# Kernel optimization log

Hardware: AMD Instinct MI355X
Metric: run time of the kernel (lower is better)

The kernel has to match this reference:

```python
import jax, jax.numpy as jnp
import numpy as np

H = 16          # num_attention_heads
GRID = 16       # crop_size // patch_size
TOK_PER_FRAME = GRID * GRID


def _rope(x, pos, dim):
    # x: (B,H,N,dim), pos: (N,) int positions
    half = dim // 2
    omega = jnp.arange(half, dtype=x.dtype) / (dim / 2.0)
    inv = 1.0 / (10000.0 ** omega)                      # (half,)
    freq = pos.astype(x.dtype)[:, None] * inv            # (N, half)
    sin = jnp.concatenate([jnp.sin(freq), jnp.sin(freq)], axis=-1)  # (N, dim)  (tile, per source)
    cos = jnp.concatenate([jnp.cos(freq), jnp.cos(freq)], axis=-1)
    y = x.reshape(*x.shape[:-1], half, 2)
    y1, y2 = y[..., 0], y[..., 1]
    rot = jnp.stack((-y2, y1), axis=-1).reshape(x.shape)  # interleaved rotate-pairs
    return x * cos + rot * sin


def _apply_3d_rope(qk, f_ids, h_ids, w_ids, d_dim):
    s = 0
    parts = []
    for pos in (f_ids, h_ids, w_ids):
        parts.append(_rope(qk[..., s:s + d_dim], pos, d_dim))
        s += d_dim
    if s < qk.shape[-1]:
        parts.append(qk[..., s:])
    return jnp.concatenate(parts, axis=-1)


def setup_inputs() -> dict:
    key = jax.random.key(0)
    ks = jax.random.split(key, 5)
    D = 1024
    B, N = 4, 2048
    sc = 0.02
    return {
        "hidden_states": jax.random.normal(ks[0], (B, N, D), jnp.float32),
        "Wq": jax.random.normal(ks[1], (D, D), jnp.float32) * sc,
        "bq": jnp.zeros((D,), jnp.float32),
        "Wk": jax.random.normal(ks[2], (D, D), jnp.float32) * sc,
        "bk": jnp.zeros((D,), jnp.float32),
        "Wv": jax.random.normal(ks[3], (D, D), jnp.float32) * sc,
        "bv": jnp.zeros((D,), jnp.float32),
        "Wo": jax.random.normal(ks[4], (D, D), jnp.float32) * sc,
        "bo": jnp.zeros((D,), jnp.float32),
    }


def reference(hidden_states, Wq, bq, Wk, bk, Wv, bv, Wo, bo):
    B, N, D = hidden_states.shape
    hd = D // H
    d_dim = 2 * (hd // 3 // 2)  # per-component rotary dim (20 for hd=64)

    def heads(x):  # (B,N,D) -> (B,H,N,hd)
        return x.reshape(B, N, H, hd).transpose(0, 2, 1, 3)

    q = heads(hidden_states @ Wq + bq)
    k = heads(hidden_states @ Wk + bk)
    v = heads(hidden_states @ Wv + bv)

    ids = jnp.arange(N)
    f_ids = ids // TOK_PER_FRAME
    rem = ids - TOK_PER_FRAME * f_ids
    h_ids = rem // GRID
    w_ids = rem - GRID * h_ids

    q = _apply_3d_rope(q, f_ids, h_ids, w_ids, d_dim)
    k = _apply_3d_rope(k, f_ids, h_ids, w_ids, d_dim)

    scale = hd ** -0.5
    attn = jnp.einsum('bhqd,bhkd->bhqk', q, k) * scale
    attn = jax.nn.softmax(attn.astype(jnp.float32), axis=-1).astype(q.dtype)
    ctx = jnp.einsum('bhqk,bhkd->bhqd', attn, v)
    ctx = ctx.transpose(0, 2, 1, 3).reshape(B, N, D)
    return ctx @ Wo + bo
```

## Files before the change

kernel.cpp:

```cpp
#include <hip/hip_runtime.h>
#include <stdint.h>

#define H_   16
#define NS_  2048
#define B_   4
#define DM_  1024
#define HD_  64
#define MTOT (B_*NS_)

typedef __attribute__((ext_vector_type(8)))  short bf16x8;
typedef __attribute__((ext_vector_type(4)))  float f32x4;
typedef __attribute__((ext_vector_type(16))) float f32x16;

__device__ __forceinline__ unsigned short f2bf(float f){
  union { float f; unsigned u; } v; v.f = f;
  unsigned r = v.u + 0x7FFFu + ((v.u >> 16) & 1u);
  return (unsigned short)(r >> 16);
}
__device__ __forceinline__ float bf2f(unsigned short u){
  union { unsigned u; float f; } v; v.u = ((unsigned)u) << 16;
  return v.f;
}
__device__ __forceinline__ unsigned pk2(float a, float b){
  return (unsigned)f2bf(a) | ((unsigned)f2bf(b) << 16);
}
__device__ __forceinline__ unsigned cvtpk(float a, float b){
  unsigned r;
  asm("v_cvt_pk_bf16_f32 %0, %1, %2" : "=v"(r) : "v"(a), "v"(b));
  return r;
}
__device__ __forceinline__ float exp2a(float x){
  float r;
  asm("v_exp_f32 %0, %1" : "=v"(r) : "v"(x));
  return r;
}
__device__ __forceinline__ void gll16(const void* g, void* l){
  __builtin_amdgcn_global_load_lds(
      (const __attribute__((address_space(1))) unsigned int*)g,
      (__attribute__((address_space(3))) unsigned int*)l,
      16, 0, 0);
}

__global__ void k_cast_x(const float* __restrict__ x, unsigned short* __restrict__ xb){
  long i = ((long)blockIdx.x*256 + threadIdx.x)*4;
  float4 v = *(const float4*)(x + i);
  ushort4 o; o.x=f2bf(v.x); o.y=f2bf(v.y); o.z=f2bf(v.z); o.w=f2bf(v.w);
  *(ushort4*)(xb + i) = o;
}

__global__ void k_wt4(const float* __restrict__ W0, const float* __restrict__ W1,
                      const float* __restrict__ W2, const float* __restrict__ W3,
                      unsigned short* __restrict__ T0, unsigned short* __restrict__ T1,
                      unsigned short* __restrict__ T2, unsigned short* __restrict__ T3){
  __shared__ float tile[64][65];
  const int z = blockIdx.z;
  const float* W = (z==0)? W0 : (z==1)? W1 : (z==2)? W2 : W3;
  unsigned short* Wt = (z==0)? T0 : (z==1)? T1 : (z==2)? T2 : T3;
  int kt = blockIdx.y*64, nt = blockIdx.x*64;
  int t = threadIdx.x;
  int r = t >> 4, c4 = (t & 15)*4;
#pragma unroll
  for (int i=0;i<4;i++){
    int k = r + i*16;
    float4 v = *(const float4*)(W + (size_t)(kt + k)*DM_ + nt + c4);
    tile[k][c4] = v.x; tile[k][c4+1]=v.y; tile[k][c4+2]=v.z; tile[k][c4+3]=v.w;
  }
  __syncthreads();
#pragma unroll
  for (int i=0;i<4;i++){
    int n = r + i*16;
    ushort4 o;
    o.x = f2bf(tile[c4+0][n]); o.y = f2bf(tile[c4+1][n]);
    o.z = f2bf(tile[c4+2][n]); o.w = f2bf(tile[c4+3][n]);
    *(ushort4*)(Wt + (size_t)(nt + n)*DM_ + kt + c4) = o;
  }
}

__global__ void k_tab(float2* __restrict__ tab){
  int n = blockIdx.x*64 + threadIdx.x;
  int f = n >> 8, rem = n & 255, hh = rem >> 4, ww = rem & 15;
  float pos[3]; pos[0]=(float)f; pos[1]=(float)hh; pos[2]=(float)ww;
#pragma unroll
  for (int c=0;c<3;c++)
#pragma unroll
    for (int i=0;i<10;i++){
      float inv = exp2f(-(float)i * 1.3287712379549449f);
      float s, co;
      sincosf(pos[c]*inv, &s, &co);
      tab[n*30 + c*10 + i] = make_float2(co, s);
    }
}

__global__ __launch_bounds__(256) void k_gemm_qkv(const unsigned short* __restrict__ A,
                                                  const unsigned short* __restrict__ wq,
                                                  const unsigned short* __restrict__ wk,
                                                  const unsigned short* __restrict__ wv,
                                                  const float* __restrict__ bq,
                                                  const float* __restrict__ bk,
                                                  const float* __restrict__ bv,
                                                  unsigned short* __restrict__ Qb,
                                                  unsigned short* __restrict__ Kb,
                                                  unsigned short* __restrict__ VTb)
{
  __shared__ unsigned short As[128*32];
  __shared__ unsigned short Bs[128*32];
  const int tid = threadIdx.x, lane = tid & 63, w = tid >> 6;
  const int mat = blockIdx.x >> 3;
  const int nt  = (blockIdx.x & 7)*128;
  const int mt  = blockIdx.y*128;
  const unsigned short* Wt  = (mat==0)? wq : (mat==1)? wk : wv;
  const float*          bias= (mat==0)? bq : (mat==1)? bk : bv;
  const int wm = (w >> 1)*64, wn = (w & 1)*64;
  const int qc = lane & 15, g = lane >> 4;
  f32x4 acc[4][4] = {};

  const unsigned short* gA = A  + (size_t)(mt + w*32 + (lane>>2))*DM_ + (lane&3)*8;
  const unsigned short* gB = Wt + (size_t)(nt + w*32 + (lane>>2))*DM_ + (lane&3)*8;
  unsigned short* lA = &As[(w*32)*32];
  unsigned short* lB = &Bs[(w*32)*32];

  for (int k0 = 0; k0 < DM_; k0 += 32){
    gll16(gA + k0,           lA);
    gll16(gA + k0 + 16*DM_,  lA + 16*32);
    gll16(gB + k0,           lB);
    gll16(gB + k0 + 16*DM_,  lB + 16*32);
    __syncthreads();
    bf16x8 af[4], bfr[4];
#pragma unroll
    for (int m=0;m<4;m++) af[m]  = *(const bf16x8*)&As[(wm + m*16 + qc)*32 + g*8];
#pragma unroll
    for (int n=0;n<4;n++) bfr[n] = *(const bf16x8*)&Bs[(wn + n*16 + qc)*32 + g*8];
#pragma unroll
    for (int m=0;m<4;m++)
#pragma unroll
      for (int n=0;n<4;n++)
        acc[m][n] = __builtin_amdgcn_mfma_f32_16x16x32_bf16(af[m], bfr[n], acc[m][n], 0,0,0);
    __syncthreads();
  }

  if (mat < 2){
    unsigned short* out = (mat==0)? Qb : Kb;
#pragma unroll
    for (int n=0;n<4;n++){
      int col = nt + wn + n*16 + qc;
      float bv_ = bias[col];
      int hh = col >> 6, d = col & 63;
#pragma unroll
      for (int m=0;m<4;m++){
#pragma unroll
        for (int r=0;r<4;r++){
          int mrow = mt + wm + m*16 + g*4 + r;
          size_t idx = (((size_t)(mrow >> 11)*H_ + hh)*NS_ + (mrow & (NS_-1)))*HD_ + d;
          out[idx] = f2bf(acc[m][n][r] + bv_);
        }
      }
    }
  } else {
#pragma unroll
    for (int n=0;n<4;n++){
      int col = nt + wn + n*16 + qc;
      float bv_ = bias[col];
      int hh = col >> 6, d = col & 63;
#pragma unroll
      for (int m=0;m<4;m++){
        int mrow0 = mt + wm + m*16 + g*4;
        int b = mrow0 >> 11, ntk = mrow0 & (NS_-1);
        int pos = (ntk & ~12) | ((ntk & 4) << 1) | ((ntk & 8) >> 1);
        ushort4 o;
        o.x = f2bf(acc[m][n][0] + bv_);
        o.y = f2bf(acc[m][n][1] + bv_);
        o.z = f2bf(acc[m][n][2] + bv_);
        o.w = f2bf(acc[m][n][3] + bv_);
        *(ushort4*)(VTb + (((size_t)(b*H_ + hh)*HD_ + d)*NS_ + pos)) = o;
      }
    }
  }
}

#define QSCALE 0.18033688011112042f
__global__ void k_rope(unsigned short* __restrict__ Qb, unsigned short* __restrict__ Kb,
                       const float2* __restrict__ tab)
{
  const int t = threadIdx.x;
  const int d4 = (t & 15)*4;
  const long gtok = (long)blockIdx.x*16 + (t >> 4);
  size_t base = (size_t)gtok*HD_ + d4;
  if (d4 >= 60){
    ushort4 v = *(ushort4*)(Qb + base);
    ushort4 o;
    o.x = f2bf(bf2f(v.x)*QSCALE); o.y = f2bf(bf2f(v.y)*QSCALE);
    o.z = f2bf(bf2f(v.z)*QSCALE); o.w = f2bf(bf2f(v.w)*QSCALE);
    *(ushort4*)(Qb + base) = o;
    return;
  }
  const int n = (int)(gtok & (NS_-1));
  const int c = d4 / 20;
  const int dd = d4 - c*20;
  const float2* tb = tab + n*30 + c*10;
  float2 cs0 = tb[(dd+0) % 10];
  float2 cs1 = tb[(dd+1) % 10];
  float2 cs2 = tb[(dd+2) % 10];
  float2 cs3 = tb[(dd+3) % 10];
#pragma unroll
  for (int which = 0; which < 2; which++){
    unsigned short* P = which ? Kb : Qb;
    float sc = which ? 1.f : QSCALE;
    ushort4 v = *(ushort4*)(P + base);
    float x0=bf2f(v.x), x1=bf2f(v.y), x2=bf2f(v.z), x3=bf2f(v.w);
    ushort4 o;
    o.x = f2bf((x0*cs0.x - x1*cs0.y)*sc);
    o.y = f2bf((x1*cs1.x + x0*cs1.y)*sc);
    o.z = f2bf((x2*cs2.x - x3*cs2.y)*sc);
    o.w = f2bf((x3*cs3.x + x2*cs3.y)*sc);
    *(ushort4*)(P + base) = o;
  }
}

__global__ __launch_bounds__(256, 4) void k_attn(const unsigned short* __restrict__ Q,
                                                 const unsigned short* __restrict__ K,
                                                 const unsigned short* __restrict__ VT,
                                                 unsigned short* __restrict__ ctxout)
{
  __shared__ __attribute__((aligned(16))) char smem[32768];
  const int tid  = threadIdx.x;
  const int lane = tid & 63, w = tid >> 6;
  const int qcol = lane & 31, h = lane >> 5;
  const int sw   = (lane & 7) << 4;
  const int bh   = blockIdx.x;
  const int q0   = blockIdx.y*128 + w*32;

  const unsigned short* Qp = Q  + ((size_t)bh*NS_ + q0)*HD_;
  const unsigned short* Kp = K  + (size_t)bh*NS_*HD_;
  const unsigned short* Vp = VT + (size_t)bh*HD_*NS_;

  const int trow = tid >> 3;
  const int tc   = (tid & 7) ^ (trow & 7);

  bf16x8 qf[4];
#pragma unroll
  for (int i=0;i<4;i++)
    qf[i] = *(const bf16x8*)(Qp + (size_t)qcol*HD_ + 16*i + 8*h);

  {
    const unsigned short* gk = Kp + (size_t)trow*HD_ + tc*8;
    const unsigned short* gv = Vp + (size_t)trow*NS_ + tc*8;
    gll16(gk,          smem + w*1024);
    gll16(gk + 32*HD_, smem + 4096 + w*1024);
    gll16(gv,          smem + 8192 + w*1024);
    gll16(gv + 32*NS_, smem + 8192 + 4096 + w*1024);
  }

  f32x16 ctx0 = {}, ctx1 = {};
  float mrun = -1e30f, lp = 0.f;

  for (int t = 0; t < NS_/64; ++t){
    const int curo = (t & 1) * 16384;
    __syncthreads();
    if (t + 1 < NS_/64){
      const int kb = (t+1)*64;
      const int nxt = ((t+1) & 1) * 16384;
      const unsigned short* gk = Kp + (size_t)(kb + trow)*HD_ + tc*8;
      const unsigned short* gv = Vp + (size_t)trow*NS_ + kb + tc*8;
      gll16(gk,          smem + nxt + w*1024);
      gll16(gk + 32*HD_, smem + nxt + 4096 + w*1024);
      gll16(gv,          smem + nxt + 8192 + w*1024);
      gll16(gv + 32*NS_, smem + nxt + 8192 + 4096 + w*1024);
    }
    const char* kls = smem + curo;
    const char* vls = smem + curo + 8192;

#pragma unroll
    for (int s = 0; s < 2; ++s){
      f32x16 st = {};
      __builtin_amdgcn_s_setprio(1);
#pragma unroll
      for (int i=0;i<4;i++){
        bf16x8 kf = *(const bf16x8*)(kls + ((((32*s + qcol)*128) + 32*i + 16*h) ^ sw));
        st = __builtin_amdgcn_mfma_f32_32x32x16_bf16(kf, qf[i], st, 0,0,0);
      }
      __builtin_amdgcn_s_setprio(0);
      float a0 = fmaxf(fmaxf(st[0],  st[1]),  st[2]);
      float a1 = fmaxf(fmaxf(st[3],  st[4]),  st[5]);
      float a2 = fmaxf(fmaxf(st[6],  st[7]),  st[8]);
      float a3 = fmaxf(fmaxf(st[9],  st[10]), st[11]);
      float a4 = fmaxf(fmaxf(st[12], st[13]), st[14]);
      float tm = fmaxf(fmaxf(fmaxf(a0,a1),a2), fmaxf(fmaxf(a3,a4),st[15]));
      if (!__all(tm - mrun <= 11.5f)){
        float tp = fmaxf(tm, __shfl_xor(tm, 32));
        float mnew = fmaxf(mrun, tp);
        float alpha = exp2a(mrun - mnew);
        lp *= alpha;
#pragma unroll
        for (int r=0;r<16;r++){ ctx0[r]*=alpha; ctx1[r]*=alpha; }
        mrun = mnew;
      }
      unsigned u[8];
      float ps = 0.f;
#pragma unroll
      for (int r=0;r<8;r++){
        float ea = exp2a(st[2*r]   - mrun);
        float eb = exp2a(st[2*r+1] - mrun);
        unsigned uu = cvtpk(ea, eb);
        u[r] = uu;
        union { unsigned q; float f; } lo, hi;
        lo.q = uu << 16; hi.q = uu & 0xFFFF0000u;
        ps += lo.f + hi.f;
      }
      lp += ps;
      bf16x8 pf0 = __builtin_bit_cast(bf16x8, make_uint4(u[0],u[1],u[2],u[3]));
      bf16x8 pf1 = __builtin_bit_cast(bf16x8, make_uint4(u[4],u[5],u[6],u[7]));

      __builtin_amdgcn_s_setprio(1);
#pragma unroll
      for (int kc=0; kc<2; ++kc){
        const bf16x8 pf = kc ? pf1 : pf0;
        bf16x8 vf0 = *(const bf16x8*)(vls + ((qcol)*128      + ((64*s + 32*kc + 16*h) ^ sw)));
        ctx0 = __builtin_amdgcn_mfma_f32_32x32x16_bf16(vf0, pf, ctx0, 0,0,0);
        bf16x8 vf1 = *(const bf16x8*)(vls + ((32 + qcol)*128 + ((64*s + 32*kc + 16*h) ^ sw)));
        ctx1 = __builtin_amdgcn_mfma_f32_32x32x16_bf16(vf1, pf, ctx1, 0,0,0);
      }
      __builtin_amdgcn_s_setprio(0);
    }
  }

  float lsum = lp + __shfl_xor(lp, 32);
  float linv = 1.f / lsum;
  __syncthreads();
  char* reg = smem + w*4096;
#pragma unroll
  for (int rq=0; rq<4; ++rq){
    int db0 = 8*rq + 4*h;
    uint2 v0, v1;
    v0.x = pk2(ctx0[4*rq+0]*linv, ctx0[4*rq+1]*linv);
    v0.y = pk2(ctx0[4*rq+2]*linv, ctx0[4*rq+3]*linv);
    v1.x = pk2(ctx1[4*rq+0]*linv, ctx1[4*rq+1]*linv);
    v1.y = pk2(ctx1[4*rq+2]*linv, ctx1[4*rq+3]*linv);
    *(uint2*)(reg + qcol*128 + db0*2)      = v0;
    *(uint2*)(reg + qcol*128 + (32+db0)*2) = v1;
  }
  __syncthreads();
  const int b = bh >> 4, head = bh & 15;
  unsigned short* outp = ctxout + ((size_t)b*NS_ + q0)*DM_ + head*HD_;
#pragma unroll
  for (int p=0;p<4;p++){
    int row = p*8 + (lane>>3);
    uint4 v = *(const uint4*)(reg + row*128 + (lane&7)*16);
    *(uint4*)(outp + (size_t)row*DM_ + (lane&7)*8) = v;
  }
}

__global__ __launch_bounds__(256) void k_gemm_o(const unsigned short* __restrict__ A,
                                                const unsigned short* __restrict__ Wt,
                                                const float* __restrict__ bias,
                                                float* __restrict__ out)
{
  __shared__ unsigned short As[128*32];
  __shared__ unsigned short Bs[128*32];
  const int tid = threadIdx.x, lane = tid & 63, w = tid >> 6;
  const int mt = blockIdx.y*128, nt = blockIdx.x*128;
  const int wm = (w >> 1)*64, wn = (w & 1)*64;
  const int qc = lane & 15, g = lane >> 4;
  f32x4 acc[4][4] = {};

  const unsigned short* gA = A  + (size_t)(mt + w*32 + (lane>>2))*DM_ + (lane&3)*8;
  const unsigned short* gB = Wt + (size_t)(nt + w*32 + (lane>>2))*DM_ + (lane&3)*8;
  unsigned short* lA = &As[(w*32)*32];
  unsigned short* lB = &Bs[(w*32)*32];

  for (int k0 = 0; k0 < DM_; k0 += 32){
    gll16(gA + k0,           lA);
    gll16(gA + k0 + 16*DM_,  lA + 16*32);
    gll16(gB + k0,           lB);
    gll16(gB + k0 + 16*DM_,  lB + 16*32);
    __syncthreads();
    bf16x8 af[4], bfr[4];
#pragma unroll
    for (int m=0;m<4;m++) af[m]  = *(const bf16x8*)&As[(wm + m*16 + qc)*32 + g*8];
#pragma unroll
    for (int n=0;n<4;n++) bfr[n] = *(const bf16x8*)&Bs[(wn + n*16 + qc)*32 + g*8];
#pragma unroll
    for (int m=0;m<4;m++)
#pragma unroll
      for (int n=0;n<4;n++)
        acc[m][n] = __builtin_amdgcn_mfma_f32_16x16x32_bf16(af[m], bfr[n], acc[m][n], 0,0,0);
    __syncthreads();
  }

#pragma unroll
  for (int n=0;n<4;n++){
    int col = nt + wn + n*16 + qc;
    float bv = bias[col];
#pragma unroll
    for (int m=0;m<4;m++){
#pragma unroll
      for (int r=0;r<4;r++){
        int mrow = mt + wm + m*16 + g*4 + r;
        out[(size_t)mrow*DM_ + col] = acc[m][n][r] + bv;
      }
    }
  }
}

extern "C" void kernel_launch(void* const* d_in, const int* in_sizes, int n_in,
                              void* d_out, int out_size, void* d_ws, size_t ws_size,
                              hipStream_t stream)
{
  const float* hs = (const float*)d_in[0];
  const float* Wq = (const float*)d_in[1];
  const float* bq = (const float*)d_in[2];
  const float* Wk = (const float*)d_in[3];
  const float* bk = (const float*)d_in[4];
  const float* Wv = (const float*)d_in[5];
  const float* bv = (const float*)d_in[6];
  const float* Wo = (const float*)d_in[7];
  const float* bo = (const float*)d_in[8];

  char* ws = (char*)d_ws;
  size_t off = 0;
  auto alloc = [&](size_t b){ void* p = ws + off; off += (b + 255) & ~(size_t)255; return p; };
  unsigned short* xb  = (unsigned short*)alloc((size_t)MTOT*DM_*2);
  unsigned short* wqt = (unsigned short*)alloc((size_t)DM_*DM_*2);
  unsigned short* wkt = (unsigned short*)alloc((size_t)DM_*DM_*2);
  unsigned short* wvt = (unsigned short*)alloc((size_t)DM_*DM_*2);
  unsigned short* wot = (unsigned short*)alloc((size_t)DM_*DM_*2);
  float2*         tab = (float2*)alloc((size_t)NS_*30*sizeof(float2));
  unsigned short* Qb  = (unsigned short*)alloc((size_t)MTOT*DM_*2);
  unsigned short* Kb  = (unsigned short*)alloc((size_t)MTOT*DM_*2);
  unsigned short* VTb = (unsigned short*)alloc((size_t)MTOT*DM_*2);
  unsigned short* cxb = (unsigned short*)alloc((size_t)MTOT*DM_*2);

  k_cast_x<<<dim3(MTOT*DM_/1024), dim3(256), 0, stream>>>(hs, xb);
  k_wt4<<<dim3(16,16,4), dim3(256), 0, stream>>>(Wq, Wk, Wv, Wo, wqt, wkt, wvt, wot);
  k_tab<<<dim3(32), dim3(64), 0, stream>>>(tab);

  k_gemm_qkv<<<dim3(24,64), dim3(256), 0, stream>>>(xb, wqt, wkt, wvt, bq, bk, bv,
                                                    Qb, Kb, VTb);

  k_rope<<<dim3(64*NS_/16), dim3(256), 0, stream>>>(Qb, Kb, tab);

  k_attn<<<dim3(64, 16), dim3(256), 0, stream>>>(Qb, Kb, VTb, cxb);

  k_gemm_o<<<dim3(8,64), dim3(256), 0, stream>>>(cxb, wot, bo, (float*)d_out);
}
```

Baseline: 248.0 us.

## Replace QKV and output GEMMs with a 256x256 double-buffered swizzled LDS GEMM

Replaces both 128x128, K=32 GEMM kernels with one templated 512-thread kernel. Each block computes a 256x256 tile with K-steps of 64, double-buffers 128KB of dynamic LDS using XOR-swizzled rows, and prefetches two stages ahead under explicit vmcnt waits and barriers. It also raises MFMA priority with setprio and remaps block IDs so neighbouring tiles land on the same XCD. The larger tiles cut global and LDS traffic per FLOP. In exchange, the grids are coarse (384 and 128 blocks), which risks poor CU occupancy and tail imbalance, and the 128 fp32 accumulators per thread risk register pressure or spills under the launch bounds.

Measured after the change: 240.0 us. 3.2% less time.

```diff
diff --git a/kernel.cpp b/kernel.cpp
--- a/kernel.cpp
+++ b/kernel.cpp
@@ -91,67 +91,150 @@
     }
 }
 
-__global__ __launch_bounds__(256) void k_gemm_qkv(const unsigned short* __restrict__ A,
-                                                  const unsigned short* __restrict__ wq,
-                                                  const unsigned short* __restrict__ wk,
-                                                  const unsigned short* __restrict__ wv,
-                                                  const float* __restrict__ bq,
-                                                  const float* __restrict__ bk,
-                                                  const float* __restrict__ bv,
-                                                  unsigned short* __restrict__ Qb,
-                                                  unsigned short* __restrict__ Kb,
-                                                  unsigned short* __restrict__ VTb)
+__device__ __forceinline__ void stage256(const unsigned short* __restrict__ gsrc,
+                                         char* ldst, int tid){
+  const int srow = tid >> 3;
+  const int gch  = (tid & 7) ^ (srow & 7);
+  const unsigned short* gp = gsrc + (size_t)srow*DM_ + gch*8;
+  char* lp = ldst + tid*16;
+#pragma unroll
+  for (int j=0;j<4;j++)
+    gll16(gp + (size_t)(j*64)*DM_, lp + j*8192);
+}
+
+template<int MODE>
+__global__ __launch_bounds__(512, 2) void k_gemm256(
+    const unsigned short* __restrict__ A,
+    const unsigned short* __restrict__ w0,
+    const unsigned short* __restrict__ w1,
+    const unsigned short* __restrict__ w2,
+    const float* __restrict__ b0,
+    const float* __restrict__ b1,
+    const float* __restrict__ b2,
+    unsigned short* __restrict__ Qb,
+    unsigned short* __restrict__ Kb,
+    unsigned short* __restrict__ VTb,
+    float* __restrict__ Fout)
 {
-  __shared__ unsigned short As[128*32];
-  __shared__ unsigned short Bs[128*32];
+  extern __shared__ char smem[];
+  char* aL = smem;
+  char* bL = smem + 65536;
   const int tid = threadIdx.x, lane = tid & 63, w = tid >> 6;
-  const int mat = blockIdx.x >> 3;
-  const int nt  = (blockIdx.x & 7)*128;
-  const int mt  = blockIdx.y*128;
-  const unsigned short* Wt  = (mat==0)? wq : (mat==1)? wk : wv;
-  const float*          bias= (mat==0)? bq : (mat==1)? bk : bv;
-  const int wm = (w >> 1)*64, wn = (w & 1)*64;
   const int qc = lane & 15, g = lane >> 4;
-  f32x4 acc[4][4] = {};
-
-  const unsigned short* gA = A  + (size_t)(mt + w*32 + (lane>>2))*DM_ + (lane&3)*8;
-  const unsigned short* gB = Wt + (size_t)(nt + w*32 + (lane>>2))*DM_ + (lane&3)*8;
-  unsigned short* lA = &As[(w*32)*32];
-  unsigned short* lB = &Bs[(w*32)*32];
-
-  for (int k0 = 0; k0 < DM_; k0 += 32){
-    gll16(gA + k0,           lA);
-    gll16(gA + k0 + 16*DM_,  lA + 16*32);
-    gll16(gB + k0,           lB);
-    gll16(gB + k0 + 16*DM_,  lB + 16*32);
-    __syncthreads();
-    bf16x8 af[4], bfr[4];
-#pragma unroll
-    for (int m=0;m<4;m++) af[m]  = *(const bf16x8*)&As[(wm + m*16 + qc)*32 + g*8];
-#pragma unroll
-    for (int n=0;n<4;n++) bfr[n] = *(const bf16x8*)&Bs[(wn + n*16 + qc)*32 + g*8];
+  const int wm = (w >> 2)*128, wn = (w & 3)*64;
+
+  int mat, mt, nt;
+  {
+    int id = blockIdx.x;
+    if (MODE == 0){
+      int wg = (id & 7)*48 + (id >> 3);
+      mat = wg >> 7; int rem = wg & 127;
+      mt = (rem >> 2)*256; nt = (rem & 3)*256;
+    } else {
+      int wg = (id & 7)*16 + (id >> 3);
+      mat = 0; mt = (wg >> 2)*256; nt = (wg & 3)*256;
+    }
+  }
+  const unsigned short* Wt = (MODE==1)? w0 : ((mat==0)? w0 : (mat==1)? w1 : w2);
+  const float* bias        = (MODE==1)? b0 : ((mat==0)? b0 : (mat==1)? b1 : b2);
+
+  const unsigned short* Ab = A  + (size_t)mt*DM_;
+  const unsigned short* Bb = Wt + (size_t)nt*DM_;
+
+  stage256(Ab,      aL,         tid);
+  stage256(Bb,      bL,         tid);
+  stage256(Ab + 64, aL + 32768, tid);
+  stage256(Bb + 64, bL + 32768, tid);
+
+  f32x4 acc[8][4] = {};
+
+  for (int kt = 0; kt < 16; ++kt){
+    const int bu = kt & 1;
+    if (kt < 15) asm volatile("s_waitcnt vmcnt(8)" ::: "memory");
+    else         asm volatile("s_waitcnt vmcnt(0)" ::: "memory");
+    __builtin_amdgcn_s_barrier();
+    __builtin_amdgcn_sched_barrier(0);
+    const char* aT = aL + bu*32768;
+    const char* bT = bL + bu*32768;
+
+    bf16x8 bfr[4][2], af[4][2], af2[4][2];
+#pragma unroll
+    for (int n=0;n<4;n++)
+#pragma unroll
+      for (int ks=0;ks<2;ks++){
+        int row = wn + n*16 + qc;
+        bfr[n][ks] = *(const bf16x8*)(bT + row*128 + ((ks*64 + g*16) ^ ((row&7)<<4)));
+      }
 #pragma unroll
     for (int m=0;m<4;m++)
 #pragma unroll
+      for (int ks=0;ks<2;ks++){
+        int row = wm + m*16 + qc;
+        af[m][ks] = *(const bf16x8*)(aT + row*128 + ((ks*64 + g*16) ^ ((row&7)<<4)));
+      }
+    __builtin_amdgcn_s_setprio(1);
+#pragma unroll
+    for (int m=0;m<4;m++)
+#pragma unroll
       for (int n=0;n<4;n++)
-        acc[m][n] = __builtin_amdgcn_mfma_f32_16x16x32_bf16(af[m], bfr[n], acc[m][n], 0,0,0);
-    __syncthreads();
-  }
-
-  if (mat < 2){
-    unsigned short* out = (mat==0)? Qb : Kb;
+#pragma unroll
+        for (int ks=0;ks<2;ks++)
+          acc[m][n] = __builtin_amdgcn_mfma_f32_16x16x32_bf16(af[m][ks], bfr[n][ks], acc[m][n], 0,0,0);
+    __builtin_amdgcn_s_setprio(0);
+#pragma unroll
+    for (int m=0;m<4;m++)
+#pragma unroll
+      for (int ks=0;ks<2;ks++){
+        int row = wm + 64 + m*16 + qc;
+        af2[m][ks] = *(const bf16x8*)(aT + row*128 + ((ks*64 + g*16) ^ ((row&7)<<4)));
+      }
+    asm volatile("s_waitcnt lgkmcnt(0)" ::: "memory");
+    __builtin_amdgcn_sched_barrier(0);
+    __builtin_amdgcn_s_barrier();
+    __builtin_amdgcn_sched_barrier(0);
+    if (kt < 14){
+      stage256(Ab + (size_t)(kt+2)*64, aL + bu*32768, tid);
+      stage256(Bb + (size_t)(kt+2)*64, bL + bu*32768, tid);
+    }
+    __builtin_amdgcn_s_setprio(1);
+#pragma unroll
+    for (int m=0;m<4;m++)
+#pragma unroll
+      for (int n=0;n<4;n++)
+#pragma unroll
+        for (int ks=0;ks<2;ks++)
+          acc[4+m][n] = __builtin_amdgcn_mfma_f32_16x16x32_bf16(af2[m][ks], bfr[n][ks], acc[4+m][n], 0,0,0);
+    __builtin_amdgcn_s_setprio(0);
+  }
+
+  if (MODE == 1){
 #pragma unroll
     for (int n=0;n<4;n++){
       int col = nt + wn + n*16 + qc;
-      float bv_ = bias[col];
+      float bv = bias[col];
+#pragma unroll
+      for (int m=0;m<8;m++){
+#pragma unroll
+        for (int r=0;r<4;r++){
+          int mrow = mt + wm + m*16 + g*4 + r;
+          Fout[(size_t)mrow*DM_ + col] = acc[m][n][r] + bv;
+        }
+      }
+    }
+  } else if (mat < 2){
+    unsigned short* out = (mat==0)? Qb : Kb;
+#pragma unroll
+    for (int n=0;n<4;n++){
+      int col = nt + wn + n*16 + qc;
+      float bv = bias[col];
       int hh = col >> 6, d = col & 63;
 #pragma unroll
-      for (int m=0;m<4;m++){
+      for (int m=0;m<8;m++){
 #pragma unroll
         for (int r=0;r<4;r++){
           int mrow = mt + wm + m*16 + g*4 + r;
           size_t idx = (((size_t)(mrow >> 11)*H_ + hh)*NS_ + (mrow & (NS_-1)))*HD_ + d;
-          out[idx] = f2bf(acc[m][n][r] + bv_);
+          out[idx] = f2bf(acc[m][n][r] + bv);
         }
       }
     }
@@ -159,18 +242,18 @@
 #pragma unroll
     for (int n=0;n<4;n++){
       int col = nt + wn + n*16 + qc;
-      float bv_ = bias[col];
+      float bv = bias[col];
       int hh = col >> 6, d = col & 63;
 #pragma unroll
-      for (int m=0;m<4;m++){
+      for (int m=0;m<8;m++){
         int mrow0 = mt + wm + m*16 + g*4;
         int b = mrow0 >> 11, ntk = mrow0 & (NS_-1);
         int pos = (ntk & ~12) | ((ntk & 4) << 1) | ((ntk & 8) >> 1);
         ushort4 o;
-        o.x = f2bf(acc[m][n][0] + bv_);
-        o.y = f2bf(acc[m][n][1] + bv_);
-        o.z = f2bf(acc[m][n][2] + bv_);
-        o.w = f2bf(acc[m][n][3] + bv_);
+        o.x = f2bf(acc[m][n][0] + bv);
+        o.y = f2bf(acc[m][n][1] + bv);
+        o.z = f2bf(acc[m][n][2] + bv);
+        o.w = f2bf(acc[m][n][3] + bv);
         *(ushort4*)(VTb + (((size_t)(b*H_ + hh)*HD_ + d)*NS_ + pos)) = o;
       }
     }
@@ -349,58 +432,6 @@
   }
 }
 
-__global__ __launch_bounds__(256) void k_gemm_o(const unsigned short* __restrict__ A,
-                                                const unsigned short* __restrict__ Wt,
-                                                const float* __restrict__ bias,
-                                                float* __restrict__ out)
-{
-  __shared__ unsigned short As[128*32];
-  __shared__ unsigned short Bs[128*32];
-  const int tid = threadIdx.x, lane = tid & 63, w = tid >> 6;
-  const int mt = blockIdx.y*128, nt = blockIdx.x*128;
-  const int wm = (w >> 1)*64, wn = (w & 1)*64;
-  const int qc = lane & 15, g = lane >> 4;
-  f32x4 acc[4][4] = {};
-
-  const unsigned short* gA = A  + (size_t)(mt + w*32 + (lane>>2))*DM_ + (lane&3)*8;
-  const unsigned short* gB = Wt + (size_t)(nt + w*32 + (lane>>2))*DM_ + (lane&3)*8;
-  unsigned short* lA = &As[(w*32)*32];
-  unsigned short* lB = &Bs[(w*32)*32];
-
-  for (int k0 = 0; k0 < DM_; k0 += 32){
-    gll16(gA + k0,           lA);
-    gll16(gA + k0 + 16*DM_,  lA + 16*32);
-    gll16(gB + k0,           lB);
-    gll16(gB + k0 + 16*DM_,  lB + 16*32);
-    __syncthreads();
-    bf16x8 af[4], bfr[4];
-#pragma unroll
-    for (int m=0;m<4;m++) af[m]  = *(const bf16x8*)&As[(wm + m*16 + qc)*32 + g*8];
-#pragma unroll
-    for (int n=0;n<4;n++) bfr[n] = *(const bf16x8*)&Bs[(wn + n*16 + qc)*32 + g*8];
-#pragma unroll
-    for (int m=0;m<4;m++)
-#pragma unroll
-      for (int n=0;n<4;n++)
-        acc[m][n] = __builtin_amdgcn_mfma_f32_16x16x32_bf16(af[m], bfr[n], acc[m][n], 0,0,0);
-    __syncthreads();
-  }
-
-#pragma unroll
-  for (int n=0;n<4;n++){
-    int col = nt + wn + n*16 + qc;
-    float bv = bias[col];
-#pragma unroll
-    for (int m=0;m<4;m++){
-#pragma unroll
-      for (int r=0;r<4;r++){
-        int mrow = mt + wm + m*16 + g*4 + r;
-        out[(size_t)mrow*DM_ + col] = acc[m][n][r] + bv;
-      }
-    }
-  }
-}
-
 extern "C" void kernel_launch(void* const* d_in, const int* in_sizes, int n_in,
                               void* d_out, int out_size, void* d_ws, size_t ws_size,
                               hipStream_t stream)
@@ -429,16 +460,23 @@
   unsigned short* VTb = (unsigned short*)alloc((size_t)MTOT*DM_*2);
   unsigned short* cxb = (unsigned short*)alloc((size_t)MTOT*DM_*2);
 
+  hipFuncSetAttribute((const void*)k_gemm256<0>,
+                      hipFuncAttributeMaxDynamicSharedMemorySize, 131072);
+  hipFuncSetAttribute((const void*)k_gemm256<1>,
+                      hipFuncAttributeMaxDynamicSharedMemorySize, 131072);
+
   k_cast_x<<<dim3(MTOT*DM_/1024), dim3(256), 0, stream>>>(hs, xb);
   k_wt4<<<dim3(16,16,4), dim3(256), 0, stream>>>(Wq, Wk, Wv, Wo, wqt, wkt, wvt, wot);
   k_tab<<<dim3(32), dim3(64), 0, stream>>>(tab);
 
-  k_gemm_qkv<<<dim3(24,64), dim3(256), 0, stream>>>(xb, wqt, wkt, wvt, bq, bk, bv,
-                                                    Qb, Kb, VTb);
+  k_gemm256<0><<<dim3(384), dim3(512), 131072, stream>>>(
+      xb, wqt, wkt, wvt, bq, bk, bv, Qb, Kb, VTb, (float*)nullptr);
 
   k_rope<<<dim3(64*NS_/16), dim3(256), 0, stream>>>(Qb, Kb, tab);
 
   k_attn<<<dim3(64, 16), dim3(256), 0, stream>>>(Qb, Kb, VTb, cxb);
 
-  k_gemm_o<<<dim3(8,64), dim3(256), 0, stream>>>(cxb, wot, bo, (float*)d_out);
-}
+  k_gemm256<1><<<dim3(128), dim3(512), 131072, stream>>>(
+      cxb, wot, nullptr, nullptr, bo, nullptr, nullptr,
+      nullptr, nullptr, nullptr, (float*)d_out);
+}
```
